# Performance work log

Measured on AMD Instinct MI355X. Metric: run time of the kernel, lower is better.

The kernel has to match this reference:

```python
import jax, jax.numpy as jnp
import numpy as np
from jax import lax

B, L, D = 2, 4096, 2048
H = 16
DK = D // H  # head qk dim == head v dim == 128
CONV = 4
EPS = 1e-5


def _causal_depthwise_conv(x, w):
    # x: [b, l, c], w: [c, K]; torch-style cross-correlation with left padding K-1
    K = w.shape[1]
    xp = jnp.pad(x, ((0, 0), (K - 1, 0), (0, 0)))
    Lx = x.shape[1]
    y = jnp.zeros_like(x)
    for i in range(K):
        y = y + xp[:, i:i + Lx, :] * w[:, i]
    return y


def _l2norm(x):
    return x / jnp.sqrt(jnp.sum(x * x, axis=-1, keepdims=True) + 1e-12)


def _delta_rule(q, k, v, beta):
    # q,k: [b,h,l,dk]; v: [b,h,l,dv]; beta: [b,h,l]
    b, h, l, dk = q.shape
    dv = v.shape[-1]
    qs = jnp.moveaxis(q, 2, 0)
    ks = jnp.moveaxis(k, 2, 0)
    vs = jnp.moveaxis(v, 2, 0)
    bs = jnp.moveaxis(beta, 2, 0)

    def step(S, inp):
        qt, kt, vt, bt = inp  # [b,h,dk],[b,h,dk],[b,h,dv],[b,h]
        kS = jnp.einsum('bhk,bhkv->bhv', kt, S)
        u = bt[..., None] * (vt - kS)
        S = S + kt[..., None] * u[:, :, None, :]
        o = jnp.einsum('bhk,bhkv->bhv', qt, S)
        return S, o

    S0 = jnp.zeros((b, h, dk, dv), dtype=q.dtype)
    _, os = lax.scan(step, S0, (qs, ks, vs, bs))
    return jnp.moveaxis(os, 0, 2)  # [b,h,l,dv]


def setup_inputs() -> dict:
    key = jax.random.key(0)
    ks = jax.random.split(key, 8)
    s = 0.02
    return {
        'hidden_states': jax.random.normal(ks[0], (B, L, D), jnp.float32),
        'w_cattn': jax.random.normal(ks[1], (D, 3 * D), jnp.float32) * s,
        'wq_conv': jax.random.normal(ks[2], (D, CONV), jnp.float32) * 0.3,
        'wk_conv': jax.random.normal(ks[3], (D, CONV), jnp.float32) * 0.3,
        'wv_conv': jax.random.normal(ks[4], (D, CONV), jnp.float32) * 0.3,
        'w_beta': jax.random.normal(ks[5], (D, H), jnp.float32) * s,
        'o_norm_w': jnp.ones((DK,), jnp.float32),
        'w_o': jax.random.normal(ks[6], (D, D), jnp.float32) * s,
    }


def reference(hidden_states, w_cattn, wq_conv, wk_conv, wv_conv, w_beta, o_norm_w, w_o):
    qkv = hidden_states @ w_cattn  # [b,l,3D]
    q, k, v = jnp.split(qkv, 3, axis=-1)
    # short conv + SiLU activation (qk_activation='silu', v conv always SiLU)
    q = jax.nn.silu(_causal_depthwise_conv(q, wq_conv))
    k = jax.nn.silu(_causal_depthwise_conv(k, wk_conv))
    v = jax.nn.silu(_causal_depthwise_conv(v, wv_conv))
    # b l (h d) -> b h l d
    def to_heads(x):
        return jnp.transpose(x.reshape(B, L, H, -1), (0, 2, 1, 3))
    q, k, v = to_heads(q), to_heads(k), to_heads(v)
    # qk_norm = 'l2'
    q = _l2norm(q)
    k = _l2norm(k)
    beta = jax.nn.sigmoid(hidden_states @ w_beta)  # [b,l,h]
    beta = jnp.transpose(beta, (0, 2, 1))  # [b,h,l]
    o = _delta_rule(q, k, v, beta)  # [b,h,l,dv]
    o = jnp.transpose(o, (0, 2, 1, 3))  # [b,l,h,dv]
    # RMSNorm over head_v_dim
    o = o * lax.rsqrt(jnp.mean(o * o, axis=-1, keepdims=True) + EPS) * o_norm_w
    o = o.reshape(B, L, D)
    return o @ w_o
```

## Files before the change

### kernel.cpp

```cpp
#include <hip/hip_runtime.h>
#include <stdint.h>

#define B_   2
#define L_   4096
#define D_   2048
#define H_   16
#define DK_  128
#define ND3  6144
#define BL_  8192

typedef __bf16 bf16x8 __attribute__((ext_vector_type(8)));
typedef float  f32x4  __attribute__((ext_vector_type(4)));

__device__ __forceinline__ float bf2f(ushort u){ return __uint_as_float(((unsigned)u)<<16); }
__device__ __forceinline__ ushort f2bf(float f){
  unsigned u = __float_as_uint(f);
  unsigned r = u + 0x7FFFu + ((u>>16)&1u);
  return (ushort)(r>>16);
}
__device__ __forceinline__ f32x4 mfma16(bf16x8 a, bf16x8 b, f32x4 c){
  return __builtin_amdgcn_mfma_f32_16x16x32_bf16(a, b, c, 0, 0, 0);
}

#define BAR_LGKM() do{ __builtin_amdgcn_sched_barrier(0); \
  asm volatile("s_waitcnt lgkmcnt(0)" ::: "memory"); \
  __builtin_amdgcn_s_barrier(); \
  __builtin_amdgcn_sched_barrier(0);}while(0)
#define BAR_VMALL() do{ __builtin_amdgcn_sched_barrier(0); \
  asm volatile("s_waitcnt vmcnt(0) lgkmcnt(0)" ::: "memory"); \
  __builtin_amdgcn_s_barrier(); \
  __builtin_amdgcn_sched_barrier(0);}while(0)

__global__ __launch_bounds__(256) void k_cast(const float* __restrict__ x, ushort* __restrict__ y, int n4){
  int i = blockIdx.x*blockDim.x + threadIdx.x;
  int stride = gridDim.x*blockDim.x;
  for (; i < n4; i += stride){
    float4 v = ((const float4*)x)[i];
    ushort4 o; o.x=f2bf(v.x); o.y=f2bf(v.y); o.z=f2bf(v.z); o.w=f2bf(v.w);
    ((ushort4*)y)[i] = o;
  }
}

__global__ __launch_bounds__(256) void k_transpose_cast(const float* __restrict__ in, ushort* __restrict__ out,
                                                        int R, int C){
  __shared__ float tile[32][33];
  int c0 = blockIdx.x*32, r0 = blockIdx.y*32;
  int tx = threadIdx.x, ty = threadIdx.y;
  #pragma unroll
  for (int i=0;i<32;i+=8) tile[ty+i][tx] = in[(size_t)(r0+ty+i)*C + (c0+tx)];
  __syncthreads();
  #pragma unroll
  for (int i=0;i<32;i+=8) out[(size_t)(c0+ty+i)*R + (r0+tx)] = f2bf(tile[tx][ty+i]);
}

template<int OUT_BF16>
__global__ __launch_bounds__(512, 1) void k_gemmks(const ushort* __restrict__ A, const ushort* __restrict__ Bt,
                                                   void* __restrict__ Cv, int M, int N, int K){
  __shared__ ushort LDSB[65536];
  char* lds = (char*)LDSB;
  const int tid = threadIdx.x, lane = tid & 63, w = tid >> 6;
  const int wm = w >> 2, wn = w & 3;
  int nwg = gridDim.x*gridDim.y;
  int id  = blockIdx.y*gridDim.x + blockIdx.x;
  int sw  = ((nwg & 7) == 0) ? ((id & 7)*(nwg >> 3) + (id >> 3)) : id;
  const int bx = sw % gridDim.x, by = sw / gridDim.x;
  const int m0 = by*256, n0 = bx*256;
  const int NT = K >> 6;
  const int NP = NT*2;
  const size_t rowb = (size_t)K*2;

  f32x4 acc[8][4];
  #pragma unroll
  for (int i=0;i<8;i++)
    #pragma unroll
    for (int j=0;j<4;j++) acc[i][j] = (f32x4){0.f,0.f,0.f,0.f};

  const int c0 = tid, c1 = tid + 512;
  const int r0c = ((c0>>6)<<4) + (c0&15), h0 = (c0>>4)&3;
  const int r1c = ((c1>>6)<<4) + (c1&15), h1 = (c1>>4)&3;
  const char* gA = (const char*)A  + (size_t)m0*rowb;
  const char* gB = (const char*)Bt + (size_t)n0*rowb;

  auto stage = [&](int slot, int tile, int s){
    const char* ga = gA + (size_t)tile*128 + s*64;
    const char* gb = gB + (size_t)tile*128 + s*64;
    char* la = lds + slot*32768;
    char* lb = la + 16384;
    __builtin_amdgcn_global_load_lds((const __attribute__((address_space(1))) void*)(ga + (size_t)r0c*rowb + h0*16),
                                     (__attribute__((address_space(3))) void*)(la + c0*16), 16, 0, 0);
    __builtin_amdgcn_global_load_lds((const __attribute__((address_space(1))) void*)(ga + (size_t)r1c*rowb + h1*16),
                                     (__attribute__((address_space(3))) void*)(la + c1*16), 16, 0, 0);
    __builtin_amdgcn_global_load_lds((const __attribute__((address_space(1))) void*)(gb + (size_t)r0c*rowb + h0*16),
                                     (__attribute__((address_space(3))) void*)(lb + c0*16), 16, 0, 0);
    __builtin_amdgcn_global_load_lds((const __attribute__((address_space(1))) void*)(gb + (size_t)r1c*rowb + h1*16),
                                     (__attribute__((address_space(3))) void*)(lb + c1*16), 16, 0, 0);
  };

  stage(0, 0, 0);
  stage(1, 0, 1);
  stage(2, 1, 0);
  __builtin_amdgcn_sched_barrier(0);
  asm volatile("s_waitcnt vmcnt(8)" ::: "memory");
  __builtin_amdgcn_s_barrier();
  __builtin_amdgcn_sched_barrier(0);

  for (int pb = 0; pb < NP; pb += 4){
    #pragma unroll
    for (int q = 0; q < 4; ++q){
      const int p = pb + q;
      const char* base = lds + q*32768;
      bf16x8 af[8], bfr[4];
      #pragma unroll
      for (int i=0;i<4;i++) af[i]  = *(const bf16x8*)(base + (wm*128 + i*16)*64 + lane*16);
      #pragma unroll
      for (int j=0;j<4;j++) bfr[j] = *(const bf16x8*)(base + 16384 + (wn*64 + j*16)*64 + lane*16);
      __builtin_amdgcn_sched_barrier(0);
      #pragma unroll
      for (int i=4;i<8;i++) af[i]  = *(const bf16x8*)(base + (wm*128 + i*16)*64 + lane*16);
      {
        int ps = p + 3;
        int tile = ps >> 1; if (tile >= NT) tile = NT - 1;
        stage(ps & 3, tile, ps & 1);
      }
      __builtin_amdgcn_sched_barrier(0);
      asm volatile("s_waitcnt lgkmcnt(4)" ::: "memory");
      __builtin_amdgcn_sched_barrier(0);
      __builtin_amdgcn_s_setprio(1);
      #pragma unroll
      for (int i=0;i<4;i++)
        #pragma unroll
        for (int j=0;j<4;j++)
          acc[i][j] = mfma16(af[i], bfr[j], acc[i][j]);
      __builtin_amdgcn_sched_barrier(0);
      asm volatile("s_waitcnt lgkmcnt(0)" ::: "memory");
      __builtin_amdgcn_sched_barrier(0);
      #pragma unroll
      for (int i=4;i<8;i++)
        #pragma unroll
        for (int j=0;j<4;j++)
          acc[i][j] = mfma16(af[i], bfr[j], acc[i][j]);
      __builtin_amdgcn_s_setprio(0);
      __builtin_amdgcn_sched_barrier(0);
      asm volatile("s_waitcnt vmcnt(8)" ::: "memory");
      __builtin_amdgcn_s_barrier();
      __builtin_amdgcn_sched_barrier(0);
    }
  }

  const int rbase = m0 + wm*128 + (lane>>4)*4;
  const int cbase = n0 + wn*64 + (lane&15);
  #pragma unroll
  for (int fi=0;fi<8;fi++)
    #pragma unroll
    for (int fj=0;fj<4;fj++)
      #pragma unroll
      for (int r=0;r<4;r++){
        int row = rbase + fi*16 + r;
        int col = cbase + fj*16;
        float v = acc[fi][fj][r];
        if (OUT_BF16) ((ushort*)Cv)[(size_t)row*N + col] = f2bf(v);
        else          ((float*) Cv)[(size_t)row*N + col] = v;
      }
}

__global__ __launch_bounds__(256) void k_wbt(const float* __restrict__ wb, ushort* __restrict__ wbT){
  int d = blockIdx.x*256 + threadIdx.x;
  #pragma unroll
  for (int h=0;h<16;h++) wbT[(size_t)h*2048 + d] = f2bf(wb[(size_t)d*16 + h]);
}

__global__ __launch_bounds__(64) void k_beta2(const ushort* __restrict__ A16, const ushort* __restrict__ wbT,
                                              float* __restrict__ beta){
  const int rt = blockIdx.x;
  const int lane = threadIdx.x;
  const int lr = lane & 15, lk8 = (lane>>4)*8;
  const int r0 = rt*16;
  f32x4 acc0 = (f32x4){0.f,0.f,0.f,0.f};
  f32x4 acc1 = (f32x4){0.f,0.f,0.f,0.f};
  for (int k0=0; k0<2048; k0+=64){
    bf16x8 a0 = *(const bf16x8*)&A16[(size_t)(r0+lr)*2048 + k0 + lk8];
    bf16x8 b0 = *(const bf16x8*)&wbT[(size_t)lr*2048 + k0 + lk8];
    bf16x8 a1 = *(const bf16x8*)&A16[(size_t)(r0+lr)*2048 + k0 + 32 + lk8];
    bf16x8 b1 = *(const bf16x8*)&wbT[(size_t)lr*2048 + k0 + 32 + lk8];
    acc0 = mfma16(a0, b0, acc0);
    acc1 = mfma16(a1, b1, acc1);
  }
  const int h = lane & 15;
  const int rbase = r0 + (lane>>4)*4;
  #pragma unroll
  for (int r=0;r<4;r++){
    int row = rbase + r;
    int b = row >> 12, l = row & 4095;
    float sg = 1.f/(1.f + __expf(-(acc0[r] + acc1[r])));
    beta[((size_t)(b*H_ + h))*L_ + l] = sg;
  }
}

__global__ __launch_bounds__(256) void k_conv2(const ushort* __restrict__ qkv,
      const float* __restrict__ wq, const float* __restrict__ wk, const float* __restrict__ wv,
      ushort* __restrict__ QH, ushort* __restrict__ KH, ushort* __restrict__ VH){
  const int seg = blockIdx.x, part = blockIdx.y, b = blockIdx.z;
  const int t = threadIdx.x;
  const int ch = t*8;
  const int h = t >> 4, d0 = (t & 15)*8;
  const float* wc = (part==0) ? wq : (part==1) ? wk : wv;
  ushort* outs = ((part==0) ? QH : (part==1) ? KH : VH)
                 + ((size_t)(b*H_ + h)*L_)*DK_ + d0;
  const ushort* inp = qkv + ((size_t)b*L_)*ND3 + part*D_ + ch;

  float wgt[4][8];
  #pragma unroll
  for (int j=0;j<8;j++){
    float4 w4 = *(const float4*)&wc[(ch + j)*4];
    wgt[0][j]=w4.x; wgt[1][j]=w4.y; wgt[2][j]=w4.z; wgt[3][j]=w4.w;
  }

  const int l0 = seg*32;
  float x0[8], x1[8], x2[8];
  {
    float* dsts[3] = {x0, x1, x2};
    #pragma unroll
    for (int i=0;i<3;i++){
      int l = l0 - 3 + i;
      float* d = dsts[i];
      if (l >= 0){
        const ushort* p = inp + (size_t)l*ND3;
        ushort4 a = *(const ushort4*)p, c = *(const ushort4*)(p+4);
        d[0]=bf2f(a.x); d[1]=bf2f(a.y); d[2]=bf2f(a.z); d[3]=bf2f(a.w);
        d[4]=bf2f(c.x); d[5]=bf2f(c.y); d[6]=bf2f(c.z); d[7]=bf2f(c.w);
      } else {
        #pragma unroll
        for (int j=0;j<8;j++) d[j] = 0.f;
      }
    }
  }

  for (int i=0;i<32;i++){
    const int l = l0 + i;
    float cur[8];
    {
      const ushort* p = inp + (size_t)l*ND3;
      ushort4 a = *(const ushort4*)p, c = *(const ushort4*)(p+4);
      cur[0]=bf2f(a.x); cur[1]=bf2f(a.y); cur[2]=bf2f(a.z); cur[3]=bf2f(a.w);
      cur[4]=bf2f(c.x); cur[5]=bf2f(c.y); cur[6]=bf2f(c.z); cur[7]=bf2f(c.w);
    }
    float y[8]; float ss = 0.f;
    #pragma unroll
    for (int j=0;j<8;j++){
      float yy = x0[j]*wgt[0][j] + x1[j]*wgt[1][j] + x2[j]*wgt[2][j] + cur[j]*wgt[3][j];
      yy = yy / (1.f + __expf(-yy));
      y[j] = yy; ss += yy*yy;
    }
    if (part < 2){
      #pragma unroll
      for (int m=1;m<16;m<<=1) ss += __shfl_xor(ss, m, 64);
      float sc = rsqrtf(ss + 1e-12f);
      #pragma unroll
      for (int j=0;j<8;j++) y[j] *= sc;
    }
    ushort4 o0, o1;
    o0.x=f2bf(y[0]); o0.y=f2bf(y[1]); o0.z=f2bf(y[2]); o0.w=f2bf(y[3]);
    o1.x=f2bf(y[4]); o1.y=f2bf(y[5]); o1.z=f2bf(y[6]); o1.w=f2bf(y[7]);
    ushort* op = outs + (size_t)l*DK_;
    *(ushort4*)op = o0; *(ushort4*)(op+4) = o1;
    #pragma unroll
    for (int j=0;j<8;j++){ x0[j]=x1[j]; x1[j]=x2[j]; x2[j]=cur[j]; }
  }
}

__global__ __launch_bounds__(64) void k_prep(const ushort* __restrict__ QH, const ushort* __restrict__ KH,
      const float* __restrict__ BETA, ushort* __restrict__ TB, ushort* __restrict__ MM,
      ushort* __restrict__ KT){
  const int bid = blockIdx.x, bh = bid>>6, c = bid&63;
  const int lane = threadIdx.x;
  __shared__ ushort Ks[64][136];
  __shared__ __align__(16) char QA[17408];
  __shared__ float bs[64];
  ushort (*Qs)[136] = (ushort (*)[136])QA;
  float  (*As)[64]  = (float  (*)[64])QA;

  const ushort* kg = KH + ((size_t)bh*L_ + c*64)*DK_;
  const ushort* qg = QH + ((size_t)bh*L_ + c*64)*DK_;
  {
    const uint4* ks4 = (const uint4*)(kg + (size_t)lane*DK_);
    const uint4* qs4 = (const uint4*)(qg + (size_t)lane*DK_);
    uint4* kd = (uint4*)&Ks[lane][0];
    uint4* qd = (uint4*)&Qs[lane][0];
    #pragma unroll
    for (int i=0;i<16;i++){ kd[i] = ks4[i]; qd[i] = qs4[i]; }
    bs[lane] = BETA[(size_t)bh*L_ + c*64 + lane];
  }
  __syncthreads();
  const int lr = lane&15, lk = lane>>4;

  f32x4 gac[4][4];
  #pragma unroll
  for (int i=0;i<4;i++)
    #pragma unroll
    for (int j=0;j<4;j++) gac[i][j] = (f32x4){0.f,0.f,0.f,0.f};
  #pragma unroll
  for (int kk=0;kk<4;kk++){
    bf16x8 fr[4];
    #pragma unroll
    for (int i=0;i<4;i++) fr[i] = *(const bf16x8*)&Ks[i*16+lr][kk*32 + lk*8];
    #pragma unroll
    for (int mi=0;mi<4;mi++)
      #pragma unroll
      for (int ni=0;ni<4;ni++)
        gac[mi][ni] = mfma16(fr[mi], fr[ni], gac[mi][ni]);
  }
  {
    f32x4 mac[4][4];
    #pragma unroll
    for (int i=0;i<4;i++)
      #pragma unroll
      for (int j=0;j<4;j++) mac[i][j] = (f32x4){0.f,0.f,0.f,0.f};
    #pragma unroll
    for (int kk=0;kk<4;kk++){
      bf16x8 frq[4], frk[4];
      #pragma unroll
      for (int i=0;i<4;i++){
        frq[i] = *(const bf16x8*)&Qs[i*16+lr][kk*32 + lk*8];
        frk[i] = *(const bf16x8*)&Ks[i*16+lr][kk*32 + lk*8];
      }
      #pragma unroll
      for (int mi=0;mi<4;mi++)
        #pragma unroll
        for (int ni=0;ni<4;ni++)
          mac[mi][ni] = mfma16(frq[mi], frk[ni], mac[mi][ni]);
    }
    #pragma unroll
    for (int mi=0;mi<4;mi++)
      #pragma unroll
      for (int ni=0;ni<4;ni++)
        #pragma unroll
        for (int r=0;r<4;r++){
          int t = mi*16 + lk*4 + r, s = ni*16 + lr;
          float v = (s <= t) ? mac[mi][ni][r] : 0.f;
          MM[(size_t)bid*4096 + t*64 + s] = f2bf(v);
        }
  }
  __syncthreads();

  #pragma unroll
  for (int mi=0;mi<4;mi++)
    #pragma unroll
    for (int ni=0;ni<4;ni++)
      #pragma unroll
      for (int r=0;r<4;r++){
        int t = mi*16 + lk*4 + r, s = ni*16 + lr;
        As[t][s] = (s < t) ? (bs[t] * gac[mi][ni][r]) : 0.f;
      }
  __syncthreads();

  float rT[64];
  #pragma unroll
  for (int t=0;t<64;t++){
    float arow = As[t][lane];
    float a = (t==lane) ? 1.f : 0.f;
    #pragma unroll
    for (int s=0;s<t;s++){
      float cc = __int_as_float(__builtin_amdgcn_readlane(__float_as_int(arow), s));
      a -= cc * rT[s];
    }
    rT[t] = a;
  }
  {
    float bc = bs[lane];
    #pragma unroll
    for (int t=0;t<64;t++)
      TB[(size_t)bid*4096 + t*64 + lane] = f2bf(rT[t] * bc);
  }
  for (int d2=0; d2<64; d2++){
    unsigned uu = *(const unsigned*)&Ks[lane][2*d2];
    KT[(size_t)bid*8192 + (size_t)(2*d2)*64 + lane]   = (ushort)(uu & 0xffffu);
    KT[(size_t)bid*8192 + (size_t)(2*d2+1)*64 + lane] = (ushort)(uu >> 16);
  }
}

template<int LRB, int GRB, int NB, int XM>
__device__ __forceinline__ void stage_swz(const ushort* __restrict__ g, ushort* l,
                                          int colOff, int w, int lane){
  for (int idx = w; idx < NB/1024; idx += 4){
    int off = idx*1024 + lane*16;
    int row = off / LRB;
    int inner = off & (LRB-1);
    int src = row*GRB + colOff + (inner ^ ((row&XM)<<4));
    __builtin_amdgcn_global_load_lds(
      (const __attribute__((address_space(1))) void*)((const char*)g + src),
      (__attribute__((address_space(3))) void*)((char*)l + idx*1024), 16, 0, 0);
  }
}

__global__ __launch_bounds__(256) void k_chunkrec(const ushort* __restrict__ QH, const ushort* __restrict__ KH,
      const ushort* __restrict__ VH, const ushort* __restrict__ TB, const ushort* __restrict__ MM,
      const ushort* __restrict__ KT, ushort* __restrict__ OH){
  const int p = blockIdx.x;
  const int xg = p & 7, s = p >> 3;
  const int bh = xg + (s >> 3)*8;
  const int vo = s & 7;
  const int tid = threadIdx.x, lane = tid&63, w = tid>>6;
  const int lr = lane&15, lk = lane>>4;
  const int tw = w*16;
  const int dw = w*32;

  __shared__ ushort SM[71680];
  ushort* Stl = SM + 67584;
  ushort* Ztl = SM + 69632;
  ushort* Utl = SM + 70656;

  const ushort* kbase  = KH + ((size_t)bh*L_)*DK_;
  const ushort* qbase  = QH + ((size_t)bh*L_)*DK_;
  const ushort* vbase  = VH + ((size_t)bh*L_)*DK_;
  const ushort* tbase  = TB + ((size_t)bh*64)*4096;
  const ushort* mbase  = MM + ((size_t)bh*64)*4096;
  const ushort* ktbase = KT + ((size_t)bh*64)*8192;
  ushort* obase = OH + ((size_t)bh*L_)*DK_ + vo*16;

  auto stageall = [&](ushort* buf, int c){
    stage_swz<256,256,16384,7>(kbase  + (size_t)c*8192, buf,         0,     w, lane);
    stage_swz<256,256,16384,7>(qbase  + (size_t)c*8192, buf + 8192,  0,     w, lane);
    stage_swz<128,128,16384,7>(ktbase + (size_t)c*8192, buf + 16384, 0,     w, lane);
    stage_swz<128,128, 8192,7>(tbase  + (size_t)c*4096, buf + 24576, 0,     w, lane);
    stage_swz<128,128, 8192,7>(mbase  + (size_t)c*4096, buf + 28672, 0,     w, lane);
    stage_swz< 32,256, 2048,0>(vbase  + (size_t)c*8192, buf + 32768, vo*32, w, lane);
  };

  f32x4 Stf[2];
  Stf[0] = (f32x4){0.f,0.f,0.f,0.f};
  Stf[1] = (f32x4){0.f,0.f,0.f,0.f};

  stageall(SM, 0);
  BAR_VMALL();

  for (int c=0; c<64; ++c){
    ushort* buf  = SM + (c&1)*33792;
    ushort* nbuf = SM + ((c+1)&1)*33792;
    const ushort* Kc  = buf;
    const ushort* Qc  = buf + 8192;
    const ushort* Ktc = buf + 16384;
    const ushort* Tbc = buf + 24576;
    const ushort* Mc  = buf + 28672;
    const ushort* Vc  = buf + 32768;

    if (c+1 < 64) stageall(nbuf, c+1);

    #pragma unroll
    for (int nd=0;nd<2;nd++)
      #pragma unroll
      for (int r=0;r<4;r++){
        int j = lk*4 + r;
        int d = dw + nd*16 + lr;
        Stl[j*128 + (d ^ ((j&7)<<3))] = f2bf(Stf[nd][r]);
      }
    BAR_LGKM();

    f32x4 xac = (f32x4){0.f,0.f,0.f,0.f};
    #pragma unroll
    for (int kk=0;kk<4;kk++){
      int e = kk*32 + lk*8;
      int ta = tw + lr;
      bf16x8 ak  = *(const bf16x8*)&Kc[ta*128 + (e ^ ((ta&7)<<3))];
      bf16x8 bst = *(const bf16x8*)&Stl[lr*128 + (e ^ ((lr&7)<<3))];
      xac = mfma16(ak, bst, xac);
    }
    #pragma unroll
    for (int r=0;r<4;r++){
      int t = tw + lk*4 + r;
      int j = lr;
      float v = bf2f(Vc[t*16 + j]);
      Ztl[j*64 + (t ^ ((j&7)<<3))] = f2bf(v - xac[r]);
    }
    BAR_LGKM();

    f32x4 uac = (f32x4){0.f,0.f,0.f,0.f};
    #pragma unroll
    for (int kk=0;kk<2;kk++){
      int e = kk*32 + lk*8;
      int ta = tw + lr;
      bf16x8 at = *(const bf16x8*)&Tbc[ta*64 + (e ^ ((ta&7)<<3))];
      bf16x8 bz = *(const bf16x8*)&Ztl[lr*64 + (e ^ ((lr&7)<<3))];
      uac = mfma16(at, bz, uac);
    }
    #pragma unroll
    for (int r=0;r<4;r++){
      int t = tw + lk*4 + r;
      int j = lr;
      Utl[j*64 + (t ^ ((j&7)<<3))] = f2bf(uac[r]);
    }
    BAR_LGKM();

    f32x4 oac = (f32x4){0.f,0.f,0.f,0.f};
    #pragma unroll
    for (int kk=0;kk<4;kk++){
      int e = kk*32 + lk*8;
      int ta = tw + lr;
      bf16x8 aq  = *(const bf16x8*)&Qc[ta*128 + (e ^ ((ta&7)<<3))];
      bf16x8 bst = *(const bf16x8*)&Stl[lr*128 + (e ^ ((lr&7)<<3))];
      oac = mfma16(aq, bst, oac);
    }
    #pragma unroll
    for (int kk=0;kk<2;kk++){
      int e = kk*32 + lk*8;
      int ta = tw + lr;
      bf16x8 am = *(const bf16x8*)&Mc[ta*64 + (e ^ ((ta&7)<<3))];
      bf16x8 bu = *(const bf16x8*)&Utl[lr*64 + (e ^ ((lr&7)<<3))];
      oac = mfma16(am, bu, oac);
    }
    #pragma unroll
    for (int r=0;r<4;r++){
      int t = tw + lk*4 + r;
      int j = lr;
      obase[(size_t)(c*64 + t)*DK_ + j] = f2bf(oac[r]);
    }

    #pragma unroll
    for (int kk=0;kk<2;kk++){
      int e = kk*32 + lk*8;
      bf16x8 au = *(const bf16x8*)&Utl[lr*64 + (e ^ ((lr&7)<<3))];
      #pragma unroll
      for (int nd=0;nd<2;nd++){
        int d = dw + nd*16 + lr;
        bf16x8 bk = *(const bf16x8*)&Ktc[d*64 + (e ^ ((d&7)<<3))];
        Stf[nd] = mfma16(au, bk, Stf[nd]);
      }
    }
    BAR_VMALL();
  }
}

__global__ __launch_bounds__(256) void k_norm(const ushort* __restrict__ OH, const float* __restrict__ gw,
                                              ushort* __restrict__ O2){
  const int blk = blockIdx.x;
  const int b = blk >> 12, l = blk & 4095;
  const int t = threadIdx.x;
  const int h = t >> 4, d0 = (t & 15) * 8;
  const ushort* ip = OH + ((size_t)(b*H_ + h)*L_ + l)*DK_ + d0;
  ushort4 a = *(const ushort4*)ip, c = *(const ushort4*)(ip+4);
  float x[8];
  x[0]=bf2f(a.x); x[1]=bf2f(a.y); x[2]=bf2f(a.z); x[3]=bf2f(a.w);
  x[4]=bf2f(c.x); x[5]=bf2f(c.y); x[6]=bf2f(c.z); x[7]=bf2f(c.w);
  float ss = 0.f;
  #pragma unroll
  for (int j=0;j<8;j++) ss += x[j]*x[j];
  #pragma unroll
  for (int m=1;m<16;m<<=1) ss += __shfl_xor(ss, m, 64);
  float sc = rsqrtf(ss * (1.f/128.f) + 1e-5f);
  ushort* opp = O2 + (size_t)blk*D_ + h*DK_ + d0;
  ushort4 o0, o1;
  o0.x=f2bf(x[0]*sc*gw[d0+0]); o0.y=f2bf(x[1]*sc*gw[d0+1]);
  o0.z=f2bf(x[2]*sc*gw[d0+2]); o0.w=f2bf(x[3]*sc*gw[d0+3]);
  o1.x=f2bf(x[4]*sc*gw[d0+4]); o1.y=f2bf(x[5]*sc*gw[d0+5]);
  o1.z=f2bf(x[6]*sc*gw[d0+6]); o1.w=f2bf(x[7]*sc*gw[d0+7]);
  *(ushort4*)opp = o0; *(ushort4*)(opp+4) = o1;
}

extern "C" void kernel_launch(void* const* d_in, const int* in_sizes, int n_in,
                              void* d_out, int out_size, void* d_ws, size_t ws_size,
                              hipStream_t stream) {
  (void)in_sizes; (void)n_in; (void)out_size; (void)ws_size;
  const float* hidden  = (const float*)d_in[0];
  const float* w_cattn = (const float*)d_in[1];
  const float* wq_conv = (const float*)d_in[2];
  const float* wk_conv = (const float*)d_in[3];
  const float* wv_conv = (const float*)d_in[4];
  const float* w_beta  = (const float*)d_in[5];
  const float* o_nw    = (const float*)d_in[6];
  const float* w_o     = (const float*)d_in[7];
  float* out = (float*)d_out;

  char* W = (char*)d_ws;
  ushort* A16   = (ushort*)(W);
  ushort* WcatT = (ushort*)(W + 33554432u);
  ushort* WoT   = (ushort*)(W + 33554432u);
  float*  BETA  = (float*) (W + 41943040u);
  ushort* WBT   = (ushort*)(W + 42467328u);
  ushort* QKV   = (ushort*)(W + 58720256u);
  ushort* TB    = (ushort*)(W + 58720256u);
  ushort* MM    = (ushort*)(W + 75497472u);
  ushort* KT    = (ushort*)(W + 92274688u);
  ushort* O2    = (ushort*)(W + 125829120u);
  ushort* QH    = (ushort*)(W + 159383552u);
  ushort* KH    = (ushort*)(W + 192937984u);
  ushort* VH    = (ushort*)(W + 226492416u);
  ushort* OH = A16;

  k_cast<<<4096, 256, 0, stream>>>(hidden, A16, (BL_*D_)/4);
  k_transpose_cast<<<dim3(ND3/32, D_/32), dim3(32,8), 0, stream>>>(w_cattn, WcatT, D_, ND3);
  k_gemmks<1><<<dim3(ND3/256, BL_/256), 512, 0, stream>>>(A16, WcatT, QKV, BL_, ND3, D_);
  k_transpose_cast<<<dim3(D_/32, D_/32), dim3(32,8), 0, stream>>>(w_o, WoT, D_, D_);
  k_wbt<<<8, 256, 0, stream>>>(w_beta, WBT);
  k_beta2<<<512, 64, 0, stream>>>(A16, WBT, BETA);
  k_conv2<<<dim3(128, 3, 2), 256, 0, stream>>>(QKV, wq_conv, wk_conv, wv_conv, QH, KH, VH);
  k_prep<<<2048, 64, 0, stream>>>(QH, KH, BETA, TB, MM, KT);
  k_chunkrec<<<256, 256, 0, stream>>>(QH, KH, VH, TB, MM, KT, OH);
  k_norm<<<BL_, 256, 0, stream>>>(OH, o_nw, O2);
  k_gemmks<0><<<dim3(D_/256, BL_/256), 512, 0, stream>>>(O2, WoT, out, BL_, D_, D_);
}
```

Measured before the change: 580.0 us.

## Restructure GEMM into double-buffered K=64 tiles split into quadrant stages

Replaces the four-slot K=32 pipeline in the bf16 GEMM with a double-buffered K=64 scheme. Each tile is split into A and B halves that are staged one at a time across four quadrant sub-steps, and each sub-step computes a 128x128 quadrant of the output. The warp-to-output mapping is changed to interleave quadrants. The aim is to overlap global-to-LDS loads with MFMA work more evenly and to use larger K per barrier. The cost is an extra barrier per sub-step and more complex wait-count logic.

```diff
diff --git a/kernel.cpp b/kernel.cpp
--- a/kernel.cpp
+++ b/kernel.cpp
@@ -54,8 +54,8 @@
 }
 
 template<int OUT_BF16>
-__global__ __launch_bounds__(512, 1) void k_gemmks(const ushort* __restrict__ A, const ushort* __restrict__ Bt,
-                                                   void* __restrict__ Cv, int M, int N, int K){
+__global__ __launch_bounds__(512, 1) void k_gemm8(const ushort* __restrict__ A, const ushort* __restrict__ Bt,
+                                                  void* __restrict__ Cv, int M, int N, int K){
   __shared__ ushort LDSB[65536];
   char* lds = (char*)LDSB;
   const int tid = threadIdx.x, lane = tid & 63, w = tid >> 6;
@@ -66,101 +66,101 @@
   const int bx = sw % gridDim.x, by = sw / gridDim.x;
   const int m0 = by*256, n0 = bx*256;
   const int NT = K >> 6;
-  const int NP = NT*2;
   const size_t rowb = (size_t)K*2;
-
-  f32x4 acc[8][4];
-  #pragma unroll
-  for (int i=0;i<8;i++)
-    #pragma unroll
-    for (int j=0;j<4;j++) acc[i][j] = (f32x4){0.f,0.f,0.f,0.f};
-
-  const int c0 = tid, c1 = tid + 512;
-  const int r0c = ((c0>>6)<<4) + (c0&15), h0 = (c0>>4)&3;
-  const int r1c = ((c1>>6)<<4) + (c1&15), h1 = (c1>>4)&3;
   const char* gA = (const char*)A  + (size_t)m0*rowb;
   const char* gB = (const char*)Bt + (size_t)n0*rowb;
 
-  auto stage = [&](int slot, int tile, int s){
-    const char* ga = gA + (size_t)tile*128 + s*64;
-    const char* gb = gB + (size_t)tile*128 + s*64;
-    char* la = lds + slot*32768;
-    char* lb = la + 16384;
-    __builtin_amdgcn_global_load_lds((const __attribute__((address_space(1))) void*)(ga + (size_t)r0c*rowb + h0*16),
-                                     (__attribute__((address_space(3))) void*)(la + c0*16), 16, 0, 0);
-    __builtin_amdgcn_global_load_lds((const __attribute__((address_space(1))) void*)(ga + (size_t)r1c*rowb + h1*16),
-                                     (__attribute__((address_space(3))) void*)(la + c1*16), 16, 0, 0);
-    __builtin_amdgcn_global_load_lds((const __attribute__((address_space(1))) void*)(gb + (size_t)r0c*rowb + h0*16),
-                                     (__attribute__((address_space(3))) void*)(lb + c0*16), 16, 0, 0);
-    __builtin_amdgcn_global_load_lds((const __attribute__((address_space(1))) void*)(gb + (size_t)r1c*rowb + h1*16),
-                                     (__attribute__((address_space(3))) void*)(lb + c1*16), 16, 0, 0);
+  f32x4 acc[8][4];
+  #pragma unroll
+  for (int i=0;i<8;i++)
+    #pragma unroll
+    for (int j=0;j<4;j++) acc[i][j] = (f32x4){0.f,0.f,0.f,0.f};
+
+  auto stage = [&](int d2, int which, int T){
+    const int isB = which >> 1, h = which & 1;
+    const char* g = isB ? gB : gA;
+    char* halfbase = lds + d2*65536 + isB*32768 + h*16384;
+    #pragma unroll
+    for (int uu=0; uu<2; ++uu){
+      int u = tid + uu*512;
+      int band = u >> 7, kk = (u >> 6) & 1, lr = u & 15, lk = (u >> 4) & 3;
+      const char* src = g + (size_t)(h*128 + band*16 + lr)*rowb + (size_t)T*128 + kk*64 + lk*16;
+      __builtin_amdgcn_global_load_lds(
+        (const __attribute__((address_space(1))) void*)src,
+        (__attribute__((address_space(3))) void*)(halfbase + u*16), 16, 0, 0);
+    }
   };
 
-  stage(0, 0, 0);
-  stage(1, 0, 1);
-  stage(2, 1, 0);
+  stage(0, 0, 0); stage(0, 1, 0); stage(0, 2, 0); stage(0, 3, 0);
+  {
+    int t1 = (1 < NT) ? 1 : 0;
+    stage(1, 0, t1); stage(1, 3, t1);
+  }
   __builtin_amdgcn_sched_barrier(0);
-  asm volatile("s_waitcnt vmcnt(8)" ::: "memory");
+  asm volatile("s_waitcnt vmcnt(4)" ::: "memory");
   __builtin_amdgcn_s_barrier();
   __builtin_amdgcn_sched_barrier(0);
 
-  for (int pb = 0; pb < NP; pb += 4){
+  for (int t = 0; t < NT; ++t){
+    const int d = t & 1;
+    const char* bufb = lds + d*65536;
+    const int tn1 = (t+1 < NT) ? t+1 : NT-1;
+    const int tn2 = (t+2 < NT) ? t+2 : NT-1;
     #pragma unroll
     for (int q = 0; q < 4; ++q){
-      const int p = pb + q;
-      const char* base = lds + q*32768;
-      bf16x8 af[8], bfr[4];
-      #pragma unroll
-      for (int i=0;i<4;i++) af[i]  = *(const bf16x8*)(base + (wm*128 + i*16)*64 + lane*16);
-      #pragma unroll
-      for (int j=0;j<4;j++) bfr[j] = *(const bf16x8*)(base + 16384 + (wn*64 + j*16)*64 + lane*16);
+      const int qm = q >> 1;
+      const int qn = (q ^ (q >> 1)) & 1;
+      bf16x8 af[4][2], bfr[2][2];
+      #pragma unroll
+      for (int il=0; il<4; ++il)
+        #pragma unroll
+        for (int kk=0; kk<2; ++kk)
+          af[il][kk] = *(const bf16x8*)(bufb + qm*16384 + ((wm*4+il)*2+kk)*1024 + lane*16);
+      #pragma unroll
+      for (int jl=0; jl<2; ++jl)
+        #pragma unroll
+        for (int kk=0; kk<2; ++kk)
+          bfr[jl][kk] = *(const bf16x8*)(bufb + 32768 + qn*16384 + ((wn*2+jl)*2+kk)*1024 + lane*16);
+      if      (q == 0) stage(d^1, 1, tn1);
+      else if (q == 1) stage(d^1, 2, tn1);
+      else if (q == 2) stage(d,   0, tn2);
+      else             stage(d,   3, tn2);
       __builtin_amdgcn_sched_barrier(0);
-      #pragma unroll
-      for (int i=4;i<8;i++) af[i]  = *(const bf16x8*)(base + (wm*128 + i*16)*64 + lane*16);
-      {
-        int ps = p + 3;
-        int tile = ps >> 1; if (tile >= NT) tile = NT - 1;
-        stage(ps & 3, tile, ps & 1);
-      }
-      __builtin_amdgcn_sched_barrier(0);
-      asm volatile("s_waitcnt lgkmcnt(4)" ::: "memory");
+      asm volatile("s_waitcnt lgkmcnt(8)" ::: "memory");
+      __builtin_amdgcn_s_barrier();
+      asm volatile("s_waitcnt lgkmcnt(0)" ::: "memory");
       __builtin_amdgcn_sched_barrier(0);
       __builtin_amdgcn_s_setprio(1);
       #pragma unroll
-      for (int i=0;i<4;i++)
+      for (int kk=0; kk<2; ++kk)
         #pragma unroll
-        for (int j=0;j<4;j++)
-          acc[i][j] = mfma16(af[i], bfr[j], acc[i][j]);
-      __builtin_amdgcn_sched_barrier(0);
-      asm volatile("s_waitcnt lgkmcnt(0)" ::: "memory");
-      __builtin_amdgcn_sched_barrier(0);
-      #pragma unroll
-      for (int i=4;i<8;i++)
-        #pragma unroll
-        for (int j=0;j<4;j++)
-          acc[i][j] = mfma16(af[i], bfr[j], acc[i][j]);
+        for (int il=0; il<4; ++il)
+          #pragma unroll
+          for (int jl=0; jl<2; ++jl)
+            acc[qm*4+il][qn*2+jl] = mfma16(af[il][kk], bfr[jl][kk], acc[qm*4+il][qn*2+jl]);
       __builtin_amdgcn_s_setprio(0);
       __builtin_amdgcn_sched_barrier(0);
-      asm volatile("s_waitcnt vmcnt(8)" ::: "memory");
+      if (q == 3){ asm volatile("s_waitcnt vmcnt(4)" ::: "memory"); }
       __builtin_amdgcn_s_barrier();
       __builtin_amdgcn_sched_barrier(0);
     }
   }
-
-  const int rbase = m0 + wm*128 + (lane>>4)*4;
-  const int cbase = n0 + wn*64 + (lane&15);
-  #pragma unroll
-  for (int fi=0;fi<8;fi++)
-    #pragma unroll
-    for (int fj=0;fj<4;fj++)
-      #pragma unroll
-      for (int r=0;r<4;r++){
-        int row = rbase + fi*16 + r;
-        int col = cbase + fj*16;
+  asm volatile("s_waitcnt vmcnt(0) lgkmcnt(0)" ::: "memory");
+
+  #pragma unroll
+  for (int fi=0; fi<8; ++fi){
+    int row0 = m0 + (fi>>2)*128 + wm*64 + (fi&3)*16 + (lane>>4)*4;
+    #pragma unroll
+    for (int fj=0; fj<4; ++fj){
+      int col = n0 + (fj>>1)*128 + wn*32 + (fj&1)*16 + (lane&15);
+      #pragma unroll
+      for (int r=0; r<4; ++r){
         float v = acc[fi][fj][r];
-        if (OUT_BF16) ((ushort*)Cv)[(size_t)row*N + col] = f2bf(v);
-        else          ((float*) Cv)[(size_t)row*N + col] = v;
+        if (OUT_BF16) ((ushort*)Cv)[(size_t)(row0+r)*N + col] = f2bf(v);
+        else          ((float*) Cv)[(size_t)(row0+r)*N + col] = v;
       }
+    }
+  }
 }
 
 __global__ __launch_bounds__(256) void k_wbt(const float* __restrict__ wb, ushort* __restrict__ wbT){
@@ -587,7 +587,7 @@
 
   k_cast<<<4096, 256, 0, stream>>>(hidden, A16, (BL_*D_)/4);
   k_transpose_cast<<<dim3(ND3/32, D_/32), dim3(32,8), 0, stream>>>(w_cattn, WcatT, D_, ND3);
-  k_gemmks<1><<<dim3(ND3/256, BL_/256), 512, 0, stream>>>(A16, WcatT, QKV, BL_, ND3, D_);
+  k_gemm8<1><<<dim3(ND3/256, BL_/256), 512, 0, stream>>>(A16, WcatT, QKV, BL_, ND3, D_);
   k_transpose_cast<<<dim3(D_/32, D_/32), dim3(32,8), 0, stream>>>(w_o, WoT, D_, D_);
   k_wbt<<<8, 256, 0, stream>>>(w_beta, WBT);
   k_beta2<<<512, 64, 0, stream>>>(A16, WBT, BETA);
@@ -595,5 +595,5 @@
   k_prep<<<2048, 64, 0, stream>>>(QH, KH, BETA, TB, MM, KT);
   k_chunkrec<<<256, 256, 0, stream>>>(QH, KH, VH, TB, MM, KT, OH);
   k_norm<<<BL_, 256, 0, stream>>>(OH, o_nw, O2);
-  k_gemmks<0><<<dim3(D_/256, BL_/256), 512, 0, stream>>>(O2, WoT, out, BL_, D_, D_);
-}
+  k_gemm8<0><<<dim3(D_/256, BL_/256), 512, 0, stream>>>(O2, WoT, out, BL_, D_, D_);
+}
```

Result: no change. 577.7 us (-0.4%).
